# Kernel tuning notes

Hardware: AMD Instinct MI355X
Metric: run time of the kernel (lower is better)

Reference implementation:

```python
import jax, jax.numpy as jnp
import numpy as np
from jax import lax

H = 1024
W = 1024
WIN = 32
STR = 16
NH = (H - WIN) // STR + 1  # 63
N = NH * NH                # 3969 patches
DN3 = ('NCDHW', 'OIDHW', 'NCDHW')
DN2 = ('NCHW', 'OIHW', 'NCHW')


def setup_inputs() -> dict:
    key = jax.random.key(0)
    ks = jax.random.split(key, 13)
    r = lambda k, s, sc=0.05: jax.random.normal(k, s, dtype=jnp.float32) * sc
    return {
        'x1': jax.random.normal(ks[0], (1, 1, 1, H, W), jnp.float32),
        'x2': jax.random.normal(ks[1], (1, 1, 1, H, W), jnp.float32),
        'conv1_w': r(ks[2], (24, 1, 2, 8, 8)),      # Conv3d(1,24,(2,8,8)) [O,I,D,H,W]
        'conv1_b': r(ks[3], (24,)),
        'conv2_w': r(ks[4], (60, 24, 5, 5)),         # Conv2d(24,60,5)
        'conv2_b': r(ks[5], (60,)),
        'deconv2_w': r(ks[6], (60, 24, 5, 5)),       # ConvTranspose2d(60,24,5) [I,O,kH,kW]
        'deconv2_b': r(ks[7], (24,)),
        'deconv1_w': r(ks[8], (24, 1, 2, 8, 8)),     # ConvTranspose3d(24,1,(2,8,8)) [I,O,D,H,W]
        'deconv1_b': r(ks[9], (1,)),
        'lin_w': r(ks[10], (N, 2), 0.5),             # per-patch Linear(2,1) weights
        'lin_b': r(ks[11], (N,), 0.5),               # per-patch Linear(2,1) bias
        'linear1_w': r(ks[12], (1, 1), 0.5),         # Linear(1,1,bias=False)
    }


def _conv(x, w, b, dn):
    nd = w.ndim - 2
    y = lax.conv_general_dilated(x, w, (1,) * nd, 'VALID', dimension_numbers=dn)
    return y + b.reshape((1, -1) + (1,) * nd)


def _convT(x, w, b, dn):
    # stride-1, pad-0 transposed conv == full-pad conv with flipped, IO-swapped kernel
    nd = w.ndim - 2
    wf = jnp.flip(w, axis=tuple(range(2, w.ndim))).swapaxes(0, 1)  # [O,I,*k]
    pad = [(k - 1, k - 1) for k in w.shape[2:]]
    y = lax.conv_general_dilated(x, wf, (1,) * nd, pad, dimension_numbers=dn)
    return y + b.reshape((1, -1) + (1,) * nd)


def reference(x1, x2, conv1_w, conv1_b, conv2_w, conv2_b, deconv2_w, deconv2_b,
              deconv1_w, deconv1_b, lin_w, lin_b, linear1_w):
    x = jnp.concatenate([x1, x2], axis=2)[0, 0]  # [2,H,W]
    idx = (jnp.arange(NH) * STR)[:, None] + jnp.arange(WIN)[None, :]  # [NH,32]
    # unfold dims 3,4 with window 32 / stride 16 -> [2,NH,NW,32,32]
    patches = x[:, idx[:, None, :, None], idx[None, :, None, :]]
    outX = patches.reshape(2, N, WIN, WIN).transpose(1, 0, 2, 3)[:, None]  # [N,1,2,32,32]
    h = jax.nn.elu(_conv(outX, conv1_w, conv1_b, DN3))        # [N,24,1,25,25]
    h = jax.nn.relu(_conv(h[:, :, 0], conv2_w, conv2_b, DN2))  # [N,60,21,21]
    h = jax.nn.elu(_convT(h, deconv2_w, deconv2_b, DN2))       # [N,24,25,25]
    h = _convT(h[:, :, None], deconv1_w, deconv1_b, DN3)       # [N,1,2,32,32]
    # per-patch Linear(2,1) over depth channels, batched over all patches
    p = jnp.einsum('nchw,nc->nhw', h[:, 0], lin_w) + lin_b[:, None, None]  # [N,32,32]
    p = p.reshape(NH, NH, WIN, WIN)
    # col2im: overlap-add fold, block 32, stride 16 -> [H,W]
    recon = jnp.zeros((H, W), jnp.float32).at[idx[:, None, :, None], idx[None, :, None, :]].add(p)
    outX2 = recon * linear1_w[0, 0]  # Linear(1,1,bias=False) per pixel
    return x2 - outX2.reshape(x2.shape)
```

## Files before the change

### kernel.cpp

```cpp
#include <hip/hip_runtime.h>
#include <hip/hip_bf16.h>

static constexpr int H_ = 1024;
static constexpr int W_ = 1024;
static constexpr int STR_ = 16;
static constexpr int NH_ = 63;
static constexpr int NPATCH_ = NH_ * NH_;
static constexpr int NGRP_ = 32;
static constexpr int NBLK_ = NH_ * NGRP_;

typedef short bf16x8 __attribute__((ext_vector_type(8)));
typedef short short4v __attribute__((ext_vector_type(4)));
typedef float f32x4 __attribute__((ext_vector_type(4)));

static constexpr int GAP16   = 49200;
static constexpr int CP0     = 49216;
static constexpr int CP1     = 55360;
static constexpr int SH2_0   = 49216;
static constexpr int SH2SZ   = 52920;
static constexpr int SH2_1   = SH2_0 + SH2SZ;
static constexpr int ZROW    = 155056;
static constexpr int H3SZ    = 30000;
static constexpr int SWC0    = 60000;
static constexpr int SWC1    = 64096;
static constexpr int SPA     = 68192;
static constexpr int LDS_BYTES = 155200;

__device__ __forceinline__ unsigned short f2bf(float x) {
    __hip_bfloat16 b = __float2bfloat16(x);
    return __builtin_bit_cast(unsigned short, b);
}

__device__ __forceinline__ f32x4 mfma_bf16(bf16x8 a, bf16x8 b, f32x4 c) {
    return __builtin_amdgcn_mfma_f32_16x16x32_bf16(a, b, c, 0, 0, 0);
}

__device__ __forceinline__ float elu_neg(float x) { return __expf(x) - 1.f; }

__global__ __launch_bounds__(1024, 4) void fused_patch_kernel(
    const float* __restrict__ x1, const float* __restrict__ x2,
    const float* __restrict__ c1b, const float* __restrict__ c2b,
    const float* __restrict__ d2b, const float* __restrict__ d1b,
    const float* __restrict__ lin_w, const float* __restrict__ lin_b,
    const unsigned short* __restrict__ w1frag,
    const unsigned short* __restrict__ w2frag,
    const unsigned short* __restrict__ dw2frag,
    const float* __restrict__ dw1,
    float* __restrict__ recon)
{
    __shared__ alignas(16) char sbuf[LDS_BYTES];
    const int b   = blockIdx.x;
    const int pi  = b / NGRP_, g = b - pi * NGRP_;
    const int pj0 = 2 * g;
    const int npat = (pj0 + 1 < NH_) ? 2 : 1;
    const int n0  = pi * NH_ + pj0;
    const int n1  = (npat == 2) ? (n0 + 1) : n0;
    const int Y0  = pi * STR_, X0 = pj0 * STR_;
    const int t   = (int)threadIdx.x;
    const int wv  = t >> 6, lane = t & 63;
    const int ln15 = lane & 15, quad = lane >> 4;

    bf16x8 w1b[8];
    #pragma unroll
    for (int gg = 0; gg < 8; ++gg)
        w1b[gg] = *(const bf16x8*)(w1frag + (gg * 64 + lane) * 8);
    const float lw00 = lin_w[2 * n0], lw01 = lin_w[2 * n0 + 1];
    const float lw10 = lin_w[2 * n1], lw11 = lin_w[2 * n1 + 1];
    const float lbn0 = lin_b[n0], lbn1 = lin_b[n1];
    const float d1b0 = d1b[0];
    const f32x4 c1bq0 = *(const f32x4*)(c1b + quad * 4);
    f32x4 c1bq1 = (f32x4){0.f, 0.f, 0.f, 0.f};
    if (quad < 2) c1bq1 = *(const f32x4*)(c1b + 16 + quad * 4);
    const f32x4 d2bq0 = *(const f32x4*)(d2b + quad * 4);
    f32x4 d2bq1 = (f32x4){0.f, 0.f, 0.f, 0.f};
    if (quad < 2) d2bq1 = *(const f32x4*)(d2b + 16 + quad * 4);
    float dwp[4] = {0.f, 0.f, 0.f, 0.f};
    {
        int r0 = t >> 5, c0 = t & 31;
        if (c0 < 24) {
            dwp[0] = dw1[(c0 * 2 + 0) * 64 + r0];
            dwp[1] = dw1[(c0 * 2 + 1) * 64 + r0];
        }
        int k1 = t + 1024, r1 = k1 >> 5, c1 = k1 & 31;
        if (c1 < 24) {
            dwp[2] = dw1[(c1 * 2 + 0) * 64 + r1];
            dwp[3] = dw1[(c1 * 2 + 1) * 64 + r1];
        }
    }

    if (t < 4)       ((float*)(sbuf + GAP16))[t] = 0.f;
    else if (t < 8)  ((float*)(sbuf + SH2_1))[t - 4] = 0.f;
    else if (t < 42) ((float*)(sbuf + ZROW))[t - 8] = 0.f;
    #pragma unroll
    for (int it = 0; it < 3; ++it) {
        int k = t + it * 1024;
        int d = (k >= 1536) ? 1 : 0;
        int rem = k - d * 1536;
        int y = rem / 48, x = rem - y * 48;
        int xg = X0 + x; if (xg > W_ - 1) xg = W_ - 1;
        unsigned short bb = f2bf((d ? x2 : x1)[(Y0 + y) * W_ + xg]);
        int row = (d * 32 + y) * 48;
        ((unsigned short*)(sbuf + CP0))[row + x] = bb;
        if (x > 0) ((unsigned short*)(sbuf + CP1))[row + x - 1] = bb;
    }
    __syncthreads();

    for (int tl = wv; tl < 65; tl += 16) {
        const int rawm = tl * 16 + ln15;
        int m = rawm; if (m > 1024) m = 1024;
        int u = m / 41, v = m - u * 41;
        const char* cps = sbuf + ((v & 1) ? CP1 : CP0);
        const int vb2 = (v & ~1) * 2;
        f32x4 acc[2];
        acc[0] = (f32x4){0.f, 0.f, 0.f, 0.f};
        acc[1] = (f32x4){0.f, 0.f, 0.f, 0.f};
        #pragma unroll
        for (int kc = 0; kc < 4; ++kc) {
            const int idx8 = kc * 4 + quad;
            const int dd = idx8 >> 3, pp = idx8 & 7;
            const unsigned int* ap = (const unsigned int*)(cps + (dd * 32 + u + pp) * 96 + vb2);
            union { unsigned int u4[4]; bf16x8 v8; } af;
            af.u4[0] = ap[0]; af.u4[1] = ap[1]; af.u4[2] = ap[2]; af.u4[3] = ap[3];
            acc[0] = mfma_bf16(w1b[kc * 2 + 0], af.v8, acc[0]);
            acc[1] = mfma_bf16(w1b[kc * 2 + 1], af.v8, acc[1]);
        }
        if (rawm < 1025) {
            char* rowp = sbuf + rawm * 48;
            short4v p0;
            #pragma unroll
            for (int r = 0; r < 4; ++r) {
                float hv = acc[0][r] + c1bq0[r];
                hv = hv > 0.f ? hv : elu_neg(hv);
                p0[r] = (short)f2bf(hv);
            }
            *(short4v*)(rowp + quad * 8) = p0;
            if (quad < 2) {
                short4v p1;
                #pragma unroll
                for (int r = 0; r < 4; ++r) {
                    float hw = acc[1][r] + c1bq1[r];
                    hw = hw > 0.f ? hw : elu_neg(hw);
                    p1[r] = (short)f2bf(hw);
                }
                *(short4v*)(rowp + 32 + quad * 8) = p1;
            }
        }
    }
    __syncthreads();

    auto s2pass = [&](int t0, int t1) {
        const bool h1 = (t1 < 56);
        int ab[2], loc[2], Pp[2];
        #pragma unroll
        for (int i = 0; i < 2; ++i) {
            int tt = i ? (h1 ? t1 : t0) : t0;
            int P = (tt >= 28) ? 1 : 0;
            int lc = tt - P * 28;
            int mm = lc * 16 + ln15; if (mm > 440) mm = 440;
            int y = mm / 21, x = mm - y * 21;
            ab[i] = (y * 41 + P * 16 + x) * 48;
            loc[i] = lc; Pp[i] = P;
        }
        f32x4 acc2[2][4];
        #pragma unroll
        for (int i = 0; i < 2; ++i)
            #pragma unroll
            for (int nt = 0; nt < 4; ++nt)
                acc2[i][nt] = (f32x4){0.f, 0.f, 0.f, 0.f};
        const unsigned short* wb = w2frag + lane * 8;
        #pragma unroll
        for (int p = 0; p < 5; ++p) {
            #pragma unroll
            for (int q = 0; q < 5; ++q) {
                const int tap  = p * 5 + q;
                const int toff = (p * 41 + q) * 48;
                bf16x8 bfr[4];
                #pragma unroll
                for (int nt = 0; nt < 4; ++nt)
                    bfr[nt] = *(const bf16x8*)(wb + (tap * 4 + nt) * 512);
                {
                    bf16x8 a = *(const bf16x8*)(sbuf + ab[0] + toff + quad * 16);
                    #pragma unroll
                    for (int nt = 0; nt < 4; ++nt)
                        acc2[0][nt] = mfma_bf16(bfr[nt], a, acc2[0][nt]);
                }
                if (h1) {
                    bf16x8 a = *(const bf16x8*)(sbuf + ab[1] + toff + quad * 16);
                    #pragma unroll
                    for (int nt = 0; nt < 4; ++nt)
                        acc2[1][nt] = mfma_bf16(bfr[nt], a, acc2[1][nt]);
                }
            }
        }
        #pragma unroll
        for (int i = 0; i < 2; ++i) {
            if (i == 1 && !h1) continue;
            int rawpix = loc[i] * 16 + ln15;
            if (rawpix < 441) {
                char* rowp = sbuf + SH2_0 + Pp[i] * SH2SZ + rawpix * 120;
                #pragma unroll
                for (int nt = 0; nt < 4; ++nt) {
                    if (nt == 3 && quad == 3) continue;
                    const f32x4 bq = *(const f32x4*)(c2b + nt * 16 + quad * 4);
                    short4v pk;
                    #pragma unroll
                    for (int r = 0; r < 4; ++r)
                        pk[r] = (short)f2bf(fmaxf(acc2[i][nt][r] + bq[r], 0.f));
                    *(short4v*)(rowp + nt * 32 + quad * 8) = pk;
                }
            }
        }
    };
    s2pass(wv, wv + 16);
    s2pass(wv + 32, wv + 48);
    __syncthreads();

    f32x4 acc3[5][2];
    {
        #pragma unroll
        for (int i = 0; i < 5; ++i) {
            acc3[i][0] = (f32x4){0.f, 0.f, 0.f, 0.f};
            acc3[i][1] = (f32x4){0.f, 0.f, 0.f, 0.f};
        }
        int uarr[5], varr[5], aoff[5];
        bool mval[5];
        #pragma unroll
        for (int i = 0; i < 5; ++i) {
            int t5 = wv + 16 * i;
            int P = (t5 >= 40) ? 1 : 0;
            int lc = t5 - P * 40;
            int m = lc * 16 + ln15;
            mval[i] = (m < 625);
            int mc = mval[i] ? m : 0;
            uarr[i] = mc / 25; varr[i] = mc - uarr[i] * 25;
            aoff[i] = SH2_0 + P * SH2SZ + (uarr[i] * 21 + varr[i]) * 120;
        }
        const unsigned short* db = dw2frag + lane * 8;
        #pragma unroll
        for (int dy = 0; dy < 5; ++dy) {
            #pragma unroll
            for (int dx = 0; dx < 5; ++dx) {
                const int tap = dy * 5 + dx;
                const int t2o = (dy * 21 + dx) * 120;
                bf16x8 bc0 = *(const bf16x8*)(db + tap * 2048);
                bf16x8 bc1 = *(const bf16x8*)(db + tap * 2048 + 512);
                bf16x8 bc2 = *(const bf16x8*)(db + tap * 2048 + 1024);
                bf16x8 bc3 = *(const bf16x8*)(db + tap * 2048 + 1536);
                #pragma unroll
                for (int i = 0; i < 5; ++i) {
                    int yv = uarr[i] - dy, xv = varr[i] - dx;
                    bool ok = mval[i] && ((unsigned)yv < 21u) && ((unsigned)xv < 21u);
                    int ra = ok ? (aoff[i] - t2o) : ZROW;
                    const char* ap = sbuf + ra + quad * 16;
                    short4v lo0 = *(const short4v*)(ap);
                    short4v hi0 = *(const short4v*)(ap + 8);
                    bf16x8 a0 = __builtin_shufflevector(lo0, hi0, 0, 1, 2, 3, 4, 5, 6, 7);
                    acc3[i][0] = mfma_bf16(bc0, a0, acc3[i][0]);
                    acc3[i][1] = mfma_bf16(bc1, a0, acc3[i][1]);
                    short4v lo1 = *(const short4v*)(ap + 64);
                    short4v hi1 = *(const short4v*)(ap + 72);
                    bf16x8 a1 = __builtin_shufflevector(lo1, hi1, 0, 1, 2, 3, 4, 5, 6, 7);
                    acc3[i][0] = mfma_bf16(bc2, a1, acc3[i][0]);
                    acc3[i][1] = mfma_bf16(bc3, a1, acc3[i][1]);
                }
            }
        }
    }
    __syncthreads();

    float* sp = (float*)(sbuf + SPA);
    {
        #pragma unroll
        for (int i = 0; i < 5; ++i) {
            int t5 = wv + 16 * i;
            int P = (t5 >= 40) ? 1 : 0;
            int lc = t5 - P * 40;
            int pix = lc * 16 + ln15;
            if (pix < 625) {
                char* rowp = sbuf + P * H3SZ + pix * 48;
                short4v p0;
                #pragma unroll
                for (int r = 0; r < 4; ++r) {
                    float hv = acc3[i][0][r] + d2bq0[r];
                    hv = hv > 0.f ? hv : elu_neg(hv);
                    p0[r] = (short)f2bf(hv);
                }
                *(short4v*)(rowp + quad * 8) = p0;
                if (quad < 2) {
                    short4v p1;
                    #pragma unroll
                    for (int r = 0; r < 4; ++r) {
                        float hw = acc3[i][1][r] + d2bq1[r];
                        hw = hw > 0.f ? hw : elu_neg(hw);
                        p1[r] = (short)f2bf(hw);
                    }
                    *(short4v*)(rowp + 32 + quad * 8) = p1;
                }
            }
        }
    }
    {
        int r0 = t >> 5, c0 = t & 31;
        ((unsigned short*)(sbuf + SWC0))[r0 * 32 + c0] = f2bf(lw00 * dwp[0] + lw01 * dwp[1]);
        ((unsigned short*)(sbuf + SWC1))[r0 * 32 + c0] = f2bf(lw10 * dwp[0] + lw11 * dwp[1]);
        int k1 = t + 1024, r1 = k1 >> 5, c1 = k1 & 31;
        ((unsigned short*)(sbuf + SWC0))[r1 * 32 + c1] = f2bf(lw00 * dwp[2] + lw01 * dwp[3]);
        ((unsigned short*)(sbuf + SWC1))[r1 * 32 + c1] = f2bf(lw10 * dwp[2] + lw11 * dwp[3]);
    }
    sp[t] = 0.f; sp[t + 1024] = 0.f;
    __syncthreads();

    {
        int qoff[4];
        #pragma unroll
        for (int r = 0; r < 4; ++r) {
            int qr = quad * 4 + r;
            qoff[r] = (qr >> 3) * 32 + (qr & 7);
        }
        #pragma unroll
        for (int i = 0; i < 5; ++i) {
            int t5 = wv + 16 * i;
            int P = (t5 >= 40) ? 1 : 0;
            int lc = t5 - P * 40;
            int rawpix = lc * 16 + ln15;
            bool pok = (rawpix < 625);
            int pc = pok ? rawpix : 624;
            bf16x8 a = *(const bf16x8*)(sbuf + P * H3SZ + pc * 48 + quad * 16);
            const char* swc = sbuf + (P ? SWC1 : SWC0);
            float* spP = sp + P * 1024;
            int uvbase = (pc / 25) * 32 + (pc % 25);
            #pragma unroll
            for (int nt = 0; nt < 4; ++nt) {
                bf16x8 wbv = *(const bf16x8*)(swc + (nt * 16 + ln15) * 64 + quad * 16);
                f32x4 acc4 = (f32x4){0.f, 0.f, 0.f, 0.f};
                acc4 = mfma_bf16(wbv, a, acc4);
                if (pok) {
                    #pragma unroll
                    for (int r = 0; r < 4; ++r)
                        atomicAdd(&spP[uvbase + nt * 64 + qoff[r]], acc4[r]);
                }
            }
        }
    }
    __syncthreads();

    {
        int yy = t >> 5, xx = t & 31;
        float ob0 = d1b0 * (lw00 + lw01) + lbn0;
        atomicAdd(&recon[(Y0 + yy) * W_ + X0 + xx], sp[t] + ob0);
        if (npat == 2) {
            float ob1 = d1b0 * (lw10 + lw11) + lbn1;
            atomicAdd(&recon[(Y0 + yy) * W_ + X0 + 16 + xx], sp[t + 1024] + ob1);
        }
    }
}

__global__ void prep_kernel(const float* __restrict__ c1w,
                            const float* __restrict__ c2w,
                            const float* __restrict__ d2w,
                            unsigned short* __restrict__ w1frag,
                            unsigned short* __restrict__ w2frag,
                            unsigned short* __restrict__ dw2frag)
{
    int i = blockIdx.x * blockDim.x + threadIdx.x;
    if (i < 51200) {
        int j = i & 7, lane = (i >> 3) & 63;
        int ln15 = lane & 15, quad = lane >> 4;
        if (i < 4096) {
            int g = i >> 9;
            int kc = g >> 1, nt = g & 1;
            int nn = nt * 16 + ln15, k = kc * 32 + quad * 8 + j;
            w1frag[i] = f2bf((nn < 24) ? c1w[nn * 128 + k] : 0.f);
        }
        {
            int nt = (i >> 9) & 3, tap = i >> 11;
            int o = nt * 16 + ln15, c = quad * 8 + j;
            float v = (o < 60 && c < 24) ? c2w[(o * 24 + c) * 25 + tap] : 0.f;
            w2frag[i] = f2bf(v);
        }
        {
            int nt = (i >> 9) & 1, kc = (i >> 10) & 1, tap = i >> 11;
            int k = kc * 32 + quad * 8 + j, c = nt * 16 + ln15;
            float v = (k < 60 && c < 24) ? d2w[(k * 24 + c) * 25 + tap] : 0.f;
            dw2frag[i] = f2bf(v);
        }
    }
}

__global__ void finalize_kernel(const float* __restrict__ x2,
                                const float* __restrict__ l1w,
                                float* __restrict__ out)
{
    int i = blockIdx.x * blockDim.x + threadIdx.x;
    if (i < H_ * W_) {
        float r = out[i];
        out[i] = x2[i] - r * l1w[0];
    }
}

extern "C" void kernel_launch(void* const* d_in, const int* in_sizes, int n_in,
                              void* d_out, int out_size, void* d_ws, size_t ws_size,
                              hipStream_t stream)
{
    const float* x1  = (const float*)d_in[0];
    const float* x2  = (const float*)d_in[1];
    const float* c1w = (const float*)d_in[2];
    const float* c1b = (const float*)d_in[3];
    const float* c2w = (const float*)d_in[4];
    const float* c2b = (const float*)d_in[5];
    const float* d2w = (const float*)d_in[6];
    const float* d2b = (const float*)d_in[7];
    const float* d1w = (const float*)d_in[8];
    const float* d1b = (const float*)d_in[9];
    const float* lw  = (const float*)d_in[10];
    const float* lb  = (const float*)d_in[11];
    const float* l1w = (const float*)d_in[12];

    float*          out     = (float*)d_out;
    unsigned short* w1frag  = (unsigned short*)d_ws;
    unsigned short* w2frag  = (unsigned short*)((char*)d_ws + 8192);
    unsigned short* dw2frag = (unsigned short*)((char*)d_ws + 110592);

    hipMemsetAsync(d_out, 0, (size_t)H_ * W_ * sizeof(float), stream);
    prep_kernel<<<100, 512, 0, stream>>>(c1w, c2w, d2w, w1frag, w2frag, dw2frag);
    fused_patch_kernel<<<NBLK_, 1024, 0, stream>>>(x1, x2, c1b, c2b, d2b, d1b,
                                                   lw, lb, w1frag, w2frag, dw2frag,
                                                   d1w, out);
    finalize_kernel<<<(H_ * W_ + 255) / 256, 256, 0, stream>>>(x2, l1w, out);
}
```

Before: 1.345 ms.

## Process one patch per block and split conv2/deconv2 into channel halves

```diff
diff --git a/kernel.cpp b/kernel.cpp
--- a/kernel.cpp
+++ b/kernel.cpp
@@ -6,25 +6,20 @@
 static constexpr int STR_ = 16;
 static constexpr int NH_ = 63;
 static constexpr int NPATCH_ = NH_ * NH_;
-static constexpr int NGRP_ = 32;
-static constexpr int NBLK_ = NH_ * NGRP_;
 
 typedef short bf16x8 __attribute__((ext_vector_type(8)));
 typedef short short4v __attribute__((ext_vector_type(4)));
 typedef float f32x4 __attribute__((ext_vector_type(4)));
 
-static constexpr int GAP16   = 49200;
-static constexpr int CP0     = 49216;
-static constexpr int CP1     = 55360;
-static constexpr int SH2_0   = 49216;
-static constexpr int SH2SZ   = 52920;
-static constexpr int SH2_1   = SH2_0 + SH2SZ;
-static constexpr int ZROW    = 155056;
-static constexpr int H3SZ    = 30000;
-static constexpr int SWC0    = 60000;
-static constexpr int SWC1    = 64096;
-static constexpr int SPA     = 68192;
-static constexpr int LDS_BYTES = 155200;
+static constexpr int GAP16 = 30000;
+static constexpr int SH2H  = 30016;
+static constexpr int SH2S  = 80;
+static constexpr int ZROW  = 65296;
+static constexpr int CP0   = 30016;
+static constexpr int CP1   = 35136;
+static constexpr int SWC   = 30016;
+static constexpr int SPA   = 34112;
+static constexpr int LDS_BYTES = 65424;
 
 __device__ __forceinline__ unsigned short f2bf(float x) {
     __hip_bfloat16 b = __float2bfloat16(x);
@@ -37,7 +32,7 @@
 
 __device__ __forceinline__ float elu_neg(float x) { return __expf(x) - 1.f; }
 
-__global__ __launch_bounds__(1024, 4) void fused_patch_kernel(
+__global__ __launch_bounds__(1024, 8) void fused_patch_kernel(
     const float* __restrict__ x1, const float* __restrict__ x2,
     const float* __restrict__ c1b, const float* __restrict__ c2b,
     const float* __restrict__ d2b, const float* __restrict__ d1b,
@@ -49,235 +44,193 @@
     float* __restrict__ recon)
 {
     __shared__ alignas(16) char sbuf[LDS_BYTES];
-    const int b   = blockIdx.x;
-    const int pi  = b / NGRP_, g = b - pi * NGRP_;
-    const int pj0 = 2 * g;
-    const int npat = (pj0 + 1 < NH_) ? 2 : 1;
-    const int n0  = pi * NH_ + pj0;
-    const int n1  = (npat == 2) ? (n0 + 1) : n0;
-    const int Y0  = pi * STR_, X0 = pj0 * STR_;
-    const int t   = (int)threadIdx.x;
-    const int wv  = t >> 6, lane = t & 63;
+    const int n  = blockIdx.x;
+    const int t  = (int)threadIdx.x;
+    const int pi = n / NH_, pj = n % NH_;
+    const int Y0 = pi * STR_, X0 = pj * STR_;
+    const int wv = t >> 6, lane = t & 63;
     const int ln15 = lane & 15, quad = lane >> 4;
 
     bf16x8 w1b[8];
     #pragma unroll
     for (int gg = 0; gg < 8; ++gg)
         w1b[gg] = *(const bf16x8*)(w1frag + (gg * 64 + lane) * 8);
-    const float lw00 = lin_w[2 * n0], lw01 = lin_w[2 * n0 + 1];
-    const float lw10 = lin_w[2 * n1], lw11 = lin_w[2 * n1 + 1];
-    const float lbn0 = lin_b[n0], lbn1 = lin_b[n1];
-    const float d1b0 = d1b[0];
-    const f32x4 c1bq0 = *(const f32x4*)(c1b + quad * 4);
-    f32x4 c1bq1 = (f32x4){0.f, 0.f, 0.f, 0.f};
-    if (quad < 2) c1bq1 = *(const f32x4*)(c1b + 16 + quad * 4);
-    const f32x4 d2bq0 = *(const f32x4*)(d2b + quad * 4);
-    f32x4 d2bq1 = (f32x4){0.f, 0.f, 0.f, 0.f};
-    if (quad < 2) d2bq1 = *(const f32x4*)(d2b + 16 + quad * 4);
-    float dwp[4] = {0.f, 0.f, 0.f, 0.f};
-    {
-        int r0 = t >> 5, c0 = t & 31;
-        if (c0 < 24) {
-            dwp[0] = dw1[(c0 * 2 + 0) * 64 + r0];
-            dwp[1] = dw1[(c0 * 2 + 1) * 64 + r0];
-        }
-        int k1 = t + 1024, r1 = k1 >> 5, c1 = k1 & 31;
-        if (c1 < 24) {
-            dwp[2] = dw1[(c1 * 2 + 0) * 64 + r1];
-            dwp[3] = dw1[(c1 * 2 + 1) * 64 + r1];
-        }
-    }
 
     if (t < 4)       ((float*)(sbuf + GAP16))[t] = 0.f;
-    else if (t < 8)  ((float*)(sbuf + SH2_1))[t - 4] = 0.f;
-    else if (t < 42) ((float*)(sbuf + ZROW))[t - 8] = 0.f;
-    #pragma unroll
-    for (int it = 0; it < 3; ++it) {
-        int k = t + it * 1024;
-        int d = (k >= 1536) ? 1 : 0;
-        int rem = k - d * 1536;
-        int y = rem / 48, x = rem - y * 48;
-        int xg = X0 + x; if (xg > W_ - 1) xg = W_ - 1;
-        unsigned short bb = f2bf((d ? x2 : x1)[(Y0 + y) * W_ + xg]);
-        int row = (d * 32 + y) * 48;
+    else if (t < 36) ((float*)(sbuf + ZROW))[t - 4] = 0.f;
+    for (int k = t; k < 2048; k += 1024) {
+        int d = k >> 10, r = k & 1023, y = r >> 5, x = r & 31;
+        unsigned short bb = f2bf((d ? x2 : x1)[(Y0 + y) * W_ + (X0 + x)]);
+        int row = (d * 32 + y) * 40;
         ((unsigned short*)(sbuf + CP0))[row + x] = bb;
         if (x > 0) ((unsigned short*)(sbuf + CP1))[row + x - 1] = bb;
     }
     __syncthreads();
 
-    for (int tl = wv; tl < 65; tl += 16) {
-        const int rawm = tl * 16 + ln15;
-        int m = rawm; if (m > 1024) m = 1024;
-        int u = m / 41, v = m - u * 41;
-        const char* cps = sbuf + ((v & 1) ? CP1 : CP0);
-        const int vb2 = (v & ~1) * 2;
-        f32x4 acc[2];
-        acc[0] = (f32x4){0.f, 0.f, 0.f, 0.f};
-        acc[1] = (f32x4){0.f, 0.f, 0.f, 0.f};
-        #pragma unroll
-        for (int kc = 0; kc < 4; ++kc) {
-            const int idx8 = kc * 4 + quad;
-            const int dd = idx8 >> 3, pp = idx8 & 7;
-            const unsigned int* ap = (const unsigned int*)(cps + (dd * 32 + u + pp) * 96 + vb2);
-            union { unsigned int u4[4]; bf16x8 v8; } af;
-            af.u4[0] = ap[0]; af.u4[1] = ap[1]; af.u4[2] = ap[2]; af.u4[3] = ap[3];
-            acc[0] = mfma_bf16(w1b[kc * 2 + 0], af.v8, acc[0]);
-            acc[1] = mfma_bf16(w1b[kc * 2 + 1], af.v8, acc[1]);
-        }
-        if (rawm < 1025) {
-            char* rowp = sbuf + rawm * 48;
-            short4v p0;
+    {
+        const f32x4 c1bq0 = *(const f32x4*)(c1b + quad * 4);
+        f32x4 c1bq1 = (f32x4){0.f, 0.f, 0.f, 0.f};
+        if (quad < 2) c1bq1 = *(const f32x4*)(c1b + 16 + quad * 4);
+        for (int tl = wv; tl < 40; tl += 16) {
+            const int rawm = tl * 16 + ln15;
+            int m = rawm > 624 ? 624 : rawm;
+            int u = m / 25, v = m - u * 25;
+            const char* cps = sbuf + ((v & 1) ? CP1 : CP0);
+            const int vb2 = (v & ~1) * 2;
+            f32x4 acc[2];
+            acc[0] = (f32x4){0.f, 0.f, 0.f, 0.f};
+            acc[1] = (f32x4){0.f, 0.f, 0.f, 0.f};
             #pragma unroll
-            for (int r = 0; r < 4; ++r) {
-                float hv = acc[0][r] + c1bq0[r];
-                hv = hv > 0.f ? hv : elu_neg(hv);
-                p0[r] = (short)f2bf(hv);
-            }
-            *(short4v*)(rowp + quad * 8) = p0;
-            if (quad < 2) {
-                short4v p1;
+            for (int kc = 0; kc < 4; ++kc) {
+                const int idx8 = kc * 4 + quad;
+                const int dd = idx8 >> 3, pp = idx8 & 7;
+                const unsigned int* ap = (const unsigned int*)(cps + (dd * 32 + u + pp) * 80 + vb2);
+                union { unsigned int u4[4]; bf16x8 v8; } af;
+                af.u4[0] = ap[0]; af.u4[1] = ap[1]; af.u4[2] = ap[2]; af.u4[3] = ap[3];
+                acc[0] = mfma_bf16(w1b[kc * 2 + 0], af.v8, acc[0]);
+                acc[1] = mfma_bf16(w1b[kc * 2 + 1], af.v8, acc[1]);
+            }
+            if (rawm < 625) {
+                char* rowp = sbuf + rawm * 48;
+                short4v p0;
                 #pragma unroll
                 for (int r = 0; r < 4; ++r) {
-                    float hw = acc[1][r] + c1bq1[r];
-                    hw = hw > 0.f ? hw : elu_neg(hw);
-                    p1[r] = (short)f2bf(hw);
-                }
-                *(short4v*)(rowp + 32 + quad * 8) = p1;
-            }
-        }
-    }
-    __syncthreads();
-
-    auto s2pass = [&](int t0, int t1) {
-        const bool h1 = (t1 < 56);
-        int ab[2], loc[2], Pp[2];
+                    float hv = acc[0][r] + c1bq0[r];
+                    hv = hv > 0.f ? hv : elu_neg(hv);
+                    p0[r] = (short)f2bf(hv);
+                }
+                *(short4v*)(rowp + quad * 8) = p0;
+                if (quad < 2) {
+                    short4v p1;
+                    #pragma unroll
+                    for (int r = 0; r < 4; ++r) {
+                        float hw = acc[1][r] + c1bq1[r];
+                        hw = hw > 0.f ? hw : elu_neg(hw);
+                        p1[r] = (short)f2bf(hw);
+                    }
+                    *(short4v*)(rowp + 32 + quad * 8) = p1;
+                }
+            }
+        }
+    }
+    __syncthreads();
+
+    int abase2[2];
+    if (wv < 14) {
         #pragma unroll
         for (int i = 0; i < 2; ++i) {
-            int tt = i ? (h1 ? t1 : t0) : t0;
-            int P = (tt >= 28) ? 1 : 0;
-            int lc = tt - P * 28;
-            int mm = lc * 16 + ln15; if (mm > 440) mm = 440;
+            int mm = (wv + i * 14) * 16 + ln15;
+            if (mm > 440) mm = 440;
             int y = mm / 21, x = mm - y * 21;
-            ab[i] = (y * 41 + P * 16 + x) * 48;
-            loc[i] = lc; Pp[i] = P;
-        }
-        f32x4 acc2[2][4];
-        #pragma unroll
-        for (int i = 0; i < 2; ++i)
-            #pragma unroll
-            for (int nt = 0; nt < 4; ++nt)
-                acc2[i][nt] = (f32x4){0.f, 0.f, 0.f, 0.f};
+            abase2[i] = (y * 25 + x) * 48;
+        }
+    }
+    f32x4 acc3[3][2];
+    int uarr[3], varr[3], aoff3[3];
+    bool mval[3];
+    #pragma unroll
+    for (int i = 0; i < 3; ++i) {
+        int m = (wv + i * 16) * 16 + ln15;
+        mval[i] = (m < 625) && !(i == 2 && wv >= 8);
+        int mc = (m < 625) ? m : 0;
+        uarr[i] = mc / 25; varr[i] = mc - uarr[i] * 25;
+        aoff3[i] = SH2H + (uarr[i] * 21 + varr[i]) * SH2S;
+    }
+
+    auto s2pass = [&](int h) {
+        if (wv >= 14) return;
+        f32x4 acc2[2][2];
+        #pragma unroll
+        for (int i = 0; i < 2; ++i) {
+            acc2[i][0] = (f32x4){0.f, 0.f, 0.f, 0.f};
+            acc2[i][1] = (f32x4){0.f, 0.f, 0.f, 0.f};
+        }
         const unsigned short* wb = w2frag + lane * 8;
         #pragma unroll
         for (int p = 0; p < 5; ++p) {
             #pragma unroll
             for (int q = 0; q < 5; ++q) {
                 const int tap  = p * 5 + q;
-                const int toff = (p * 41 + q) * 48;
-                bf16x8 bfr[4];
-                #pragma unroll
-                for (int nt = 0; nt < 4; ++nt)
-                    bfr[nt] = *(const bf16x8*)(wb + (tap * 4 + nt) * 512);
-                {
-                    bf16x8 a = *(const bf16x8*)(sbuf + ab[0] + toff + quad * 16);
-                    #pragma unroll
-                    for (int nt = 0; nt < 4; ++nt)
-                        acc2[0][nt] = mfma_bf16(bfr[nt], a, acc2[0][nt]);
-                }
-                if (h1) {
-                    bf16x8 a = *(const bf16x8*)(sbuf + ab[1] + toff + quad * 16);
-                    #pragma unroll
-                    for (int nt = 0; nt < 4; ++nt)
-                        acc2[1][nt] = mfma_bf16(bfr[nt], a, acc2[1][nt]);
+                const int toff = (p * 25 + q) * 48;
+                bf16x8 b0 = *(const bf16x8*)(wb + (tap * 4 + 2 * h + 0) * 512);
+                bf16x8 b1 = *(const bf16x8*)(wb + (tap * 4 + 2 * h + 1) * 512);
+                #pragma unroll
+                for (int i = 0; i < 2; ++i) {
+                    bf16x8 a = *(const bf16x8*)(sbuf + abase2[i] + toff + quad * 16);
+                    acc2[i][0] = mfma_bf16(b0, a, acc2[i][0]);
+                    acc2[i][1] = mfma_bf16(b1, a, acc2[i][1]);
                 }
             }
         }
         #pragma unroll
         for (int i = 0; i < 2; ++i) {
-            if (i == 1 && !h1) continue;
-            int rawpix = loc[i] * 16 + ln15;
+            int rawpix = (wv + i * 14) * 16 + ln15;
             if (rawpix < 441) {
-                char* rowp = sbuf + SH2_0 + Pp[i] * SH2SZ + rawpix * 120;
-                #pragma unroll
-                for (int nt = 0; nt < 4; ++nt) {
-                    if (nt == 3 && quad == 3) continue;
-                    const f32x4 bq = *(const f32x4*)(c2b + nt * 16 + quad * 4);
+                char* rowp = sbuf + SH2H + rawpix * SH2S;
+                #pragma unroll
+                for (int lnt = 0; lnt < 2; ++lnt) {
+                    if (h == 1 && lnt == 1 && quad == 3) continue;
+                    const f32x4 bq = *(const f32x4*)(c2b + h * 32 + lnt * 16 + quad * 4);
                     short4v pk;
                     #pragma unroll
                     for (int r = 0; r < 4; ++r)
-                        pk[r] = (short)f2bf(fmaxf(acc2[i][nt][r] + bq[r], 0.f));
-                    *(short4v*)(rowp + nt * 32 + quad * 8) = pk;
+                        pk[r] = (short)f2bf(fmaxf(acc2[i][lnt][r] + bq[r], 0.f));
+                    *(short4v*)(rowp + lnt * 32 + quad * 8) = pk;
                 }
             }
         }
     };
-    s2pass(wv, wv + 16);
-    s2pass(wv + 32, wv + 48);
-    __syncthreads();
-
-    f32x4 acc3[5][2];
-    {
-        #pragma unroll
-        for (int i = 0; i < 5; ++i) {
-            acc3[i][0] = (f32x4){0.f, 0.f, 0.f, 0.f};
-            acc3[i][1] = (f32x4){0.f, 0.f, 0.f, 0.f};
-        }
-        int uarr[5], varr[5], aoff[5];
-        bool mval[5];
-        #pragma unroll
-        for (int i = 0; i < 5; ++i) {
-            int t5 = wv + 16 * i;
-            int P = (t5 >= 40) ? 1 : 0;
-            int lc = t5 - P * 40;
-            int m = lc * 16 + ln15;
-            mval[i] = (m < 625);
-            int mc = mval[i] ? m : 0;
-            uarr[i] = mc / 25; varr[i] = mc - uarr[i] * 25;
-            aoff[i] = SH2_0 + P * SH2SZ + (uarr[i] * 21 + varr[i]) * 120;
-        }
-        const unsigned short* db = dw2frag + lane * 8;
+
+    auto s3pass = [&](int h) {
+        const unsigned short* db = dw2frag + lane * 8 + h * 1024;
         #pragma unroll
         for (int dy = 0; dy < 5; ++dy) {
             #pragma unroll
             for (int dx = 0; dx < 5; ++dx) {
                 const int tap = dy * 5 + dx;
-                const int t2o = (dy * 21 + dx) * 120;
-                bf16x8 bc0 = *(const bf16x8*)(db + tap * 2048);
-                bf16x8 bc1 = *(const bf16x8*)(db + tap * 2048 + 512);
-                bf16x8 bc2 = *(const bf16x8*)(db + tap * 2048 + 1024);
-                bf16x8 bc3 = *(const bf16x8*)(db + tap * 2048 + 1536);
-                #pragma unroll
-                for (int i = 0; i < 5; ++i) {
+                const int t2o = (dy * 21 + dx) * SH2S;
+                bf16x8 b0 = *(const bf16x8*)(db + tap * 2048);
+                bf16x8 b1 = *(const bf16x8*)(db + tap * 2048 + 512);
+                #pragma unroll
+                for (int i = 0; i < 3; ++i) {
+                    if (i == 2 && wv >= 8) continue;
                     int yv = uarr[i] - dy, xv = varr[i] - dx;
                     bool ok = mval[i] && ((unsigned)yv < 21u) && ((unsigned)xv < 21u);
-                    int ra = ok ? (aoff[i] - t2o) : ZROW;
-                    const char* ap = sbuf + ra + quad * 16;
-                    short4v lo0 = *(const short4v*)(ap);
-                    short4v hi0 = *(const short4v*)(ap + 8);
-                    bf16x8 a0 = __builtin_shufflevector(lo0, hi0, 0, 1, 2, 3, 4, 5, 6, 7);
-                    acc3[i][0] = mfma_bf16(bc0, a0, acc3[i][0]);
-                    acc3[i][1] = mfma_bf16(bc1, a0, acc3[i][1]);
-                    short4v lo1 = *(const short4v*)(ap + 64);
-                    short4v hi1 = *(const short4v*)(ap + 72);
-                    bf16x8 a1 = __builtin_shufflevector(lo1, hi1, 0, 1, 2, 3, 4, 5, 6, 7);
-                    acc3[i][0] = mfma_bf16(bc2, a1, acc3[i][0]);
-                    acc3[i][1] = mfma_bf16(bc3, a1, acc3[i][1]);
-                }
-            }
-        }
-    }
-    __syncthreads();
-
+                    int ra = ok ? (aoff3[i] - t2o) : ZROW;
+                    bf16x8 a = *(const bf16x8*)(sbuf + ra + quad * 16);
+                    acc3[i][0] = mfma_bf16(b0, a, acc3[i][0]);
+                    acc3[i][1] = mfma_bf16(b1, a, acc3[i][1]);
+                }
+            }
+        }
+    };
+
+    s2pass(0);
+    #pragma unroll
+    for (int i = 0; i < 3; ++i) {
+        acc3[i][0] = (f32x4){0.f, 0.f, 0.f, 0.f};
+        acc3[i][1] = (f32x4){0.f, 0.f, 0.f, 0.f};
+    }
+    __syncthreads();
+    s3pass(0);
+    __syncthreads();
+    s2pass(1);
+    __syncthreads();
+    s3pass(1);
+    __syncthreads();
+
+    const float lw0 = lin_w[2 * n], lw1 = lin_w[2 * n + 1];
     float* sp = (float*)(sbuf + SPA);
     {
-        #pragma unroll
-        for (int i = 0; i < 5; ++i) {
-            int t5 = wv + 16 * i;
-            int P = (t5 >= 40) ? 1 : 0;
-            int lc = t5 - P * 40;
-            int pix = lc * 16 + ln15;
+        const f32x4 d2bq0 = *(const f32x4*)(d2b + quad * 4);
+        f32x4 d2bq1 = (f32x4){0.f, 0.f, 0.f, 0.f};
+        if (quad < 2) d2bq1 = *(const f32x4*)(d2b + 16 + quad * 4);
+        #pragma unroll
+        for (int i = 0; i < 3; ++i) {
+            if (i == 2 && wv >= 8) continue;
+            int pix = (wv + i * 16) * 16 + ln15;
             if (pix < 625) {
-                char* rowp = sbuf + P * H3SZ + pix * 48;
+                char* rowp = sbuf + pix * 48;
                 short4v p0;
                 #pragma unroll
                 for (int r = 0; r < 4; ++r) {
@@ -301,13 +254,21 @@
     }
     {
         int r0 = t >> 5, c0 = t & 31;
-        ((unsigned short*)(sbuf + SWC0))[r0 * 32 + c0] = f2bf(lw00 * dwp[0] + lw01 * dwp[1]);
-        ((unsigned short*)(sbuf + SWC1))[r0 * 32 + c0] = f2bf(lw10 * dwp[0] + lw11 * dwp[1]);
+        float a0 = 0.f, a1 = 0.f;
+        if (c0 < 24) {
+            a0 = dw1[(c0 * 2 + 0) * 64 + r0];
+            a1 = dw1[(c0 * 2 + 1) * 64 + r0];
+        }
+        ((unsigned short*)(sbuf + SWC))[r0 * 32 + c0] = f2bf(lw0 * a0 + lw1 * a1);
         int k1 = t + 1024, r1 = k1 >> 5, c1 = k1 & 31;
-        ((unsigned short*)(sbuf + SWC0))[r1 * 32 + c1] = f2bf(lw00 * dwp[2] + lw01 * dwp[3]);
-        ((unsigned short*)(sbuf + SWC1))[r1 * 32 + c1] = f2bf(lw10 * dwp[2] + lw11 * dwp[3]);
-    }
-    sp[t] = 0.f; sp[t + 1024] = 0.f;
+        float b0v = 0.f, b1v = 0.f;
+        if (c1 < 24) {
+            b0v = dw1[(c1 * 2 + 0) * 64 + r1];
+            b1v = dw1[(c1 * 2 + 1) * 64 + r1];
+        }
+        ((unsigned short*)(sbuf + SWC))[r1 * 32 + c1] = f2bf(lw0 * b0v + lw1 * b1v);
+    }
+    sp[t] = 0.f;
     __syncthreads();
 
     {
@@ -318,40 +279,33 @@
             qoff[r] = (qr >> 3) * 32 + (qr & 7);
         }
         #pragma unroll
-        for (int i = 0; i < 5; ++i) {
-            int t5 = wv + 16 * i;
-            int P = (t5 >= 40) ? 1 : 0;
-            int lc = t5 - P * 40;
-            int rawpix = lc * 16 + ln15;
+        for (int i = 0; i < 3; ++i) {
+            int mt = wv + i * 16;
+            if (mt >= 40) continue;
+            int rawpix = mt * 16 + ln15;
             bool pok = (rawpix < 625);
             int pc = pok ? rawpix : 624;
-            bf16x8 a = *(const bf16x8*)(sbuf + P * H3SZ + pc * 48 + quad * 16);
-            const char* swc = sbuf + (P ? SWC1 : SWC0);
-            float* spP = sp + P * 1024;
+            bf16x8 a = *(const bf16x8*)(sbuf + pc * 48 + quad * 16);
             int uvbase = (pc / 25) * 32 + (pc % 25);
             #pragma unroll
             for (int nt = 0; nt < 4; ++nt) {
-                bf16x8 wbv = *(const bf16x8*)(swc + (nt * 16 + ln15) * 64 + quad * 16);
+                bf16x8 wbv = *(const bf16x8*)(sbuf + SWC + (nt * 16 + ln15) * 64 + quad * 16);
                 f32x4 acc4 = (f32x4){0.f, 0.f, 0.f, 0.f};
                 acc4 = mfma_bf16(wbv, a, acc4);
                 if (pok) {
                     #pragma unroll
                     for (int r = 0; r < 4; ++r)
-                        atomicAdd(&spP[uvbase + nt * 64 + qoff[r]], acc4[r]);
-                }
-            }
-        }
-    }
-    __syncthreads();
-
-    {
+                        atomicAdd(&sp[uvbase + nt * 64 + qoff[r]], acc4[r]);
+                }
+            }
+        }
+    }
+    __syncthreads();
+
+    {
+        const float obias = d1b[0] * (lw0 + lw1) + lin_b[n];
         int yy = t >> 5, xx = t & 31;
-        float ob0 = d1b0 * (lw00 + lw01) + lbn0;
-        atomicAdd(&recon[(Y0 + yy) * W_ + X0 + xx], sp[t] + ob0);
-        if (npat == 2) {
-            float ob1 = d1b0 * (lw10 + lw11) + lbn1;
-            atomicAdd(&recon[(Y0 + yy) * W_ + X0 + 16 + xx], sp[t + 1024] + ob1);
-        }
+        atomicAdd(&recon[(Y0 + yy) * W_ + X0 + xx], sp[t] + obias);
     }
 }
 
@@ -423,8 +377,8 @@
 
     hipMemsetAsync(d_out, 0, (size_t)H_ * W_ * sizeof(float), stream);
     prep_kernel<<<100, 512, 0, stream>>>(c1w, c2w, d2w, w1frag, w2frag, dw2frag);
-    fused_patch_kernel<<<NBLK_, 1024, 0, stream>>>(x1, x2, c1b, c2b, d2b, d1b,
-                                                   lw, lb, w1frag, w2frag, dw2frag,
-                                                   d1w, out);
+    fused_patch_kernel<<<NPATCH_, 1024, 0, stream>>>(x1, x2, c1b, c2b, d2b, d1b,
+                                                     lw, lb, w1frag, w2frag, dw2frag,
+                                                     d1w, out);
     finalize_kernel<<<(H_ * W_ + 255) / 256, 256, 0, stream>>>(x2, l1w, out);
 }
```

New measurement: 1.525 ms. 13.4% more time.
